# Kernel optimization log

Measured on AMD Instinct MI355X. Metric: run time of the kernel, lower is better.

The kernel has to match this reference:

```python
import math
import jax, jax.numpy as jnp
import numpy as np

UNITS = 256
D_IN = 256
BATCH = 65536
STRENGTH = 0.5
PERIOD = 25.0
LAMBDA_SLOW = 0.1
JITTER = 0.05
H_INERTIA = 0.9
REST_BASELINE = 1.0


def setup_inputs() -> dict:
    key = jax.random.key(0)
    k1, k2, k3, k4, k5, k6 = jax.random.split(key, 6)
    glorot = math.sqrt(2.0 / (D_IN + UNITS))
    return {
        "inputs": jax.random.normal(k1, (BATCH, D_IN), dtype=jnp.float32),
        "prev_h": jax.random.normal(k2, (BATCH, UNITS), dtype=jnp.float32),
        "prev_G": jax.random.normal(k3, (BATCH, UNITS), dtype=jnp.float32),
        "prev_phase": jax.random.normal(k4, (BATCH, 1), dtype=jnp.float32),
        "w_in": jax.random.normal(k5, (D_IN, UNITS), dtype=jnp.float32) * glorot,
        "w_rec": jax.random.normal(k6, (UNITS, UNITS), dtype=jnp.float32) * (1.0 / math.sqrt(UNITS)),
        "bias": jnp.zeros((UNITS,), dtype=jnp.float32),
    }


def reference(inputs, prev_h, prev_G, prev_phase, w_in, w_rec, bias):
    half = UNITS // 2
    # roll-like swap of the two halves of the hidden state
    raw_signal = jnp.concatenate([prev_h[:, half:], prev_h[:, :half]], axis=1)
    # slow exponential-moving-average field
    new_G = (1.0 - LAMBDA_SLOW) * prev_G + LAMBDA_SLOW * raw_signal
    mean = jnp.mean(new_G, axis=-1, keepdims=True)
    std = jnp.std(new_G, axis=-1, keepdims=True)  # population std, matches tf.math.reduce_std
    G_norm = (new_G - mean) / (std + 1e-6)
    new_phase = prev_phase + 2.0 * math.pi / PERIOD
    oscillator = jnp.sin(new_phase)
    bias_signal = jnp.mean(raw_signal, axis=-1, keepdims=True) - 0.1
    combined_signal = oscillator + JITTER * bias_signal
    field_effect = REST_BASELINE + STRENGTH * combined_signal * jnp.tanh(G_norm)
    z = (inputs @ w_in + prev_h @ w_rec + bias) * field_effect
    h = H_INERTIA * prev_h + (1.0 - H_INERTIA) * jax.nn.elu(z)
    h = jnp.clip(h, -20.0, 20.0)
    return (h, new_G, new_phase)
```

## Files before the change

kernel.cpp:

```cpp
#include <hip/hip_runtime.h>

typedef unsigned short ushort_t;
typedef short v8s __attribute__((ext_vector_type(8)));
typedef float v4f __attribute__((ext_vector_type(4)));

#define BATCH    65536
#define UNITS    256
#define M_TILE   32
#define A_PAD    33
#define GT_STRIDE 264
#define LDS_A    0
#define LDS_A_SZ (64 * A_PAD * 16)
#define LDS_GT   LDS_A_SZ
#define LDS_GT_SZ (32 * GT_STRIDE * 2)
#define LDS_SC   (LDS_GT + LDS_GT_SZ)
#define LDS_TOT  (LDS_SC + 1408)

__device__ __forceinline__ float b2f(ushort_t u) {
    union { unsigned int i; float f; } v; v.i = ((unsigned int)u) << 16; return v.f;
}
__device__ __forceinline__ ushort_t f2b(float f) {
    union { float f; unsigned int i; } v; v.f = f;
    unsigned int r = (v.i + 0x7fffu + ((v.i >> 16) & 1u)) >> 16;
    return (ushort_t)r;
}

__global__ void pack_w(const float* __restrict__ w_in,
                       const float* __restrict__ w_rec,
                       ushort_t* __restrict__ Wp) {
    int gid = blockIdx.x * 256 + threadIdx.x;
    int k = gid >> 8, n = gid & 255;
    float v = (k < 256) ? w_in[k * 256 + n] : w_rec[(k - 256) * 256 + n];
    int s = k >> 5, t = n >> 4;
    int lane = ((k >> 3) & 3) * 16 + (n & 15);
    Wp[(size_t)(((s * 16 + t) * 64) + lane) * 8 + (k & 7)] = f2b(v);
}

__global__ __launch_bounds__(256, 3)
void fused_cell(const float* __restrict__ inputs,
                const float* __restrict__ prev_h,
                const float* __restrict__ prev_G,
                const float* __restrict__ prev_phase,
                const ushort_t* __restrict__ Wp,
                const float* __restrict__ bias,
                float* __restrict__ out) {
    __shared__ __align__(16) char smem[LDS_TOT];
    short* Ak     = (short*)(smem + LDS_A);
    short* Gt     = (short*)(smem + LDS_GT);
    float* r_mean = (float*)(smem + LDS_SC);
    float* r_rstd = r_mean + 32;
    float* r_comb = r_rstd + 32;
    float* bias_f = r_comb + 32;

    const int tid  = threadIdx.x;
    const int row0 = blockIdx.x * M_TILE;

    float* outH = out;
    float* outG = out + (size_t)BATCH * UNITS;
    float* outP = out + (size_t)2 * BATCH * UNITS;

    bias_f[tid] = bias[tid];

    {
        const int lr = tid >> 3;
        const int p  = tid & 7;
        const int gr = row0 + lr;
        float s1 = 0.f, s2 = 0.f, sh = 0.f;
        #pragma unroll
        for (int i = 0; i < 8; ++i) {
            int c0 = i * 32 + p * 4;
            int pc = (c0 + 128) & 255;
            float4 xi = *(const float4*)(inputs + (size_t)gr * UNITS + c0);
            float4 hp = *(const float4*)(prev_h + (size_t)gr * UNITS + pc);
            float4 gp = *(const float4*)(prev_G + (size_t)gr * UNITS + c0);
            ushort4 xq; xq.x = f2b(xi.x); xq.y = f2b(xi.y); xq.z = f2b(xi.z); xq.w = f2b(xi.w);
            *(ushort4*)(Ak + ((c0 >> 3) * A_PAD + lr) * 8 + (c0 & 7)) = xq;
            ushort4 hq; hq.x = f2b(hp.x); hq.y = f2b(hp.y); hq.z = f2b(hp.z); hq.w = f2b(hp.w);
            int kh = 256 + pc;
            *(ushort4*)(Ak + ((kh >> 3) * A_PAD + lr) * 8 + (pc & 7)) = hq;
            float4 ng;
            ng.x = 0.9f * gp.x + 0.1f * hp.x;
            ng.y = 0.9f * gp.y + 0.1f * hp.y;
            ng.z = 0.9f * gp.z + 0.1f * hp.z;
            ng.w = 0.9f * gp.w + 0.1f * hp.w;
            s1 += ng.x + ng.y + ng.z + ng.w;
            s2 += ng.x*ng.x + ng.y*ng.y + ng.z*ng.z + ng.w*ng.w;
            sh += hp.x + hp.y + hp.z + hp.w;
            *(float4*)(outG + (size_t)gr * UNITS + c0) = ng;
            ushort4 gq; gq.x = f2b(ng.x); gq.y = f2b(ng.y); gq.z = f2b(ng.z); gq.w = f2b(ng.w);
            *(ushort4*)(Gt + lr * GT_STRIDE + c0) = gq;
        }
        #pragma unroll
        for (int off = 4; off > 0; off >>= 1) {
            s1 += __shfl_xor(s1, off, 64);
            s2 += __shfl_xor(s2, off, 64);
            sh += __shfl_xor(sh, off, 64);
        }
        if (p == 0) {
            float mean = s1 * (1.f / 256.f);
            float var  = s2 * (1.f / 256.f) - mean * mean;
            float rstd = 1.f / (sqrtf(fmaxf(var, 0.f)) + 1e-6f);
            float np   = prev_phase[gr] + 0.2513274122871834591f;
            outP[gr] = np;
            float comb = sinf(np) + 0.05f * (sh * (1.f / 256.f) - 0.1f);
            r_mean[lr] = mean; r_rstd[lr] = rstd; r_comb[lr] = comb;
        }
    }

    __syncthreads();

    const int l   = tid & 63;
    const int w   = tid >> 6;
    const int n16 = l & 15;
    const int q   = l >> 4;

    v4f acc[2][4];
    const v4f z4 = {0.f, 0.f, 0.f, 0.f};
    #pragma unroll
    for (int mi = 0; mi < 2; ++mi)
        #pragma unroll
        for (int t = 0; t < 4; ++t) acc[mi][t] = z4;

    const short* ap = Ak + (q * A_PAD + n16) * 8;
    const short* bw = (const short*)Wp + ((size_t)(w * 4) * 64 + l) * 8;

    #pragma unroll 2
    for (int s = 0; s < 16; ++s) {
        v8s a0 = *(const v8s*)(ap + s * (4 * A_PAD * 8));
        v8s a1 = *(const v8s*)(ap + s * (4 * A_PAD * 8) + 128);
        #pragma unroll
        for (int t = 0; t < 4; ++t) {
            v8s b = *(const v8s*)(bw + (s * 16 + t) * 512);
            acc[0][t] = __builtin_amdgcn_mfma_f32_16x16x32_bf16(a0, b, acc[0][t], 0, 0, 0);
            acc[1][t] = __builtin_amdgcn_mfma_f32_16x16x32_bf16(a1, b, acc[1][t], 0, 0, 0);
        }
    }

    #pragma unroll
    for (int mi = 0; mi < 2; ++mi) {
        #pragma unroll
        for (int t = 0; t < 4; ++t) {
            int c = (w * 4 + t) * 16 + n16;
            float bz = bias_f[c];
            #pragma unroll
            for (int r = 0; r < 4; ++r) {
                int lr = mi * 16 + q * 4 + r;
                int gr = row0 + lr;
                float gval = b2f((ushort_t)Gt[lr * GT_STRIDE + c]);
                float gn = (gval - r_mean[lr]) * r_rstd[lr];
                float e2 = __expf(2.f * gn);
                float th = 1.f - 2.f / (e2 + 1.f);
                float field = 1.f + 0.5f * r_comb[lr] * th;
                float z = (acc[mi][t][r] + bz) * field;
                float el = (z > 0.f) ? z : (__expf(z) - 1.f);
                int kh = 256 + c;
                float hprev = b2f((ushort_t)Ak[((kh >> 3) * A_PAD + lr) * 8 + (c & 7)]);
                float h = 0.9f * hprev + 0.1f * el;
                h = fminf(fmaxf(h, -20.f), 20.f);
                outH[(size_t)gr * UNITS + c] = h;
            }
        }
    }
}

extern "C" void kernel_launch(void* const* d_in, const int* in_sizes, int n_in,
                              void* d_out, int out_size, void* d_ws, size_t ws_size,
                              hipStream_t stream) {
    const float* inputs     = (const float*)d_in[0];
    const float* prev_h     = (const float*)d_in[1];
    const float* prev_G     = (const float*)d_in[2];
    const float* prev_phase = (const float*)d_in[3];
    const float* w_in       = (const float*)d_in[4];
    const float* w_rec      = (const float*)d_in[5];
    const float* bias       = (const float*)d_in[6];
    float* out    = (float*)d_out;
    ushort_t* Wp  = (ushort_t*)d_ws;

    pack_w<<<512, 256, 0, stream>>>(w_in, w_rec, Wp);
    fused_cell<<<BATCH / M_TILE, 256, 0, stream>>>(inputs, prev_h, prev_G,
                                                   prev_phase, Wp, bias, out);
}
```

Before: 318.1 us.

## Load input activations directly into MFMA registers and shrink LDS A buffer

The input-activation half of the A operand is no longer staged through LDS. Each lane loads fp32 inputs from global memory straight into the MFMA fragment layout, converts them to bf16 in registers, and prefetches the first input and weight fragments before the prologue. This halves the A staging buffer in LDS, so occupancy can rise to 4 blocks per CU, and it removes the LDS write/read traffic for that half. The outputs are now written with nontemporal stores. In exchange, the per-lane global loads of inputs are less coalesced (32-byte chunks spread across rows), the fully unrolled loop adds register pressure, and bf16 conversion now happens inside the MFMA loop.

Measured after the change: 317.2 us. About the same (-0.3%).

```diff
diff --git a/kernel.cpp b/kernel.cpp
--- a/kernel.cpp
+++ b/kernel.cpp
@@ -9,9 +9,9 @@
 #define M_TILE   32
 #define A_PAD    33
 #define GT_STRIDE 264
-#define LDS_A    0
-#define LDS_A_SZ (64 * A_PAD * 16)
-#define LDS_GT   LDS_A_SZ
+#define LDS_AK   0
+#define LDS_AK_SZ (32 * A_PAD * 16)
+#define LDS_GT   LDS_AK_SZ
 #define LDS_GT_SZ (32 * GT_STRIDE * 2)
 #define LDS_SC   (LDS_GT + LDS_GT_SZ)
 #define LDS_TOT  (LDS_SC + 1408)
@@ -36,7 +36,7 @@
     Wp[(size_t)(((s * 16 + t) * 64) + lane) * 8 + (k & 7)] = f2b(v);
 }
 
-__global__ __launch_bounds__(256, 3)
+__global__ __launch_bounds__(256, 4)
 void fused_cell(const float* __restrict__ inputs,
                 const float* __restrict__ prev_h,
                 const float* __restrict__ prev_G,
@@ -45,7 +45,7 @@
                 const float* __restrict__ bias,
                 float* __restrict__ out) {
     __shared__ __align__(16) char smem[LDS_TOT];
-    short* Ak     = (short*)(smem + LDS_A);
+    short* Ak     = (short*)(smem + LDS_AK);
     short* Gt     = (short*)(smem + LDS_GT);
     float* r_mean = (float*)(smem + LDS_SC);
     float* r_rstd = r_mean + 32;
@@ -61,6 +61,23 @@
 
     bias_f[tid] = bias[tid];
 
+    const int l   = tid & 63;
+    const int w   = tid >> 6;
+    const int n16 = l & 15;
+    const int q   = l >> 4;
+
+    const float* ainp0 = inputs + (size_t)(row0 + n16) * UNITS + q * 8;
+    const float* ainp1 = ainp0 + 16 * UNITS;
+    const short* bw    = (const short*)Wp + ((size_t)(w * 4) * 64 + l) * 8;
+
+    float4 pA00 = *(const float4*)(ainp0);
+    float4 pA01 = *(const float4*)(ainp0 + 4);
+    float4 pA10 = *(const float4*)(ainp1);
+    float4 pA11 = *(const float4*)(ainp1 + 4);
+    v8s pB[4];
+    #pragma unroll
+    for (int tt = 0; tt < 4; ++tt) pB[tt] = *(const v8s*)(bw + tt * 512);
+
     {
         const int lr = tid >> 3;
         const int p  = tid & 7;
@@ -70,14 +87,8 @@
         for (int i = 0; i < 8; ++i) {
             int c0 = i * 32 + p * 4;
             int pc = (c0 + 128) & 255;
-            float4 xi = *(const float4*)(inputs + (size_t)gr * UNITS + c0);
             float4 hp = *(const float4*)(prev_h + (size_t)gr * UNITS + pc);
             float4 gp = *(const float4*)(prev_G + (size_t)gr * UNITS + c0);
-            ushort4 xq; xq.x = f2b(xi.x); xq.y = f2b(xi.y); xq.z = f2b(xi.z); xq.w = f2b(xi.w);
-            *(ushort4*)(Ak + ((c0 >> 3) * A_PAD + lr) * 8 + (c0 & 7)) = xq;
-            ushort4 hq; hq.x = f2b(hp.x); hq.y = f2b(hp.y); hq.z = f2b(hp.z); hq.w = f2b(hp.w);
-            int kh = 256 + pc;
-            *(ushort4*)(Ak + ((kh >> 3) * A_PAD + lr) * 8 + (pc & 7)) = hq;
             float4 ng;
             ng.x = 0.9f * gp.x + 0.1f * hp.x;
             ng.y = 0.9f * gp.y + 0.1f * hp.y;
@@ -86,9 +97,12 @@
             s1 += ng.x + ng.y + ng.z + ng.w;
             s2 += ng.x*ng.x + ng.y*ng.y + ng.z*ng.z + ng.w*ng.w;
             sh += hp.x + hp.y + hp.z + hp.w;
-            *(float4*)(outG + (size_t)gr * UNITS + c0) = ng;
+            v4f ngv; ngv[0] = ng.x; ngv[1] = ng.y; ngv[2] = ng.z; ngv[3] = ng.w;
+            __builtin_nontemporal_store(ngv, (v4f*)(outG + (size_t)gr * UNITS + c0));
             ushort4 gq; gq.x = f2b(ng.x); gq.y = f2b(ng.y); gq.z = f2b(ng.z); gq.w = f2b(ng.w);
             *(ushort4*)(Gt + lr * GT_STRIDE + c0) = gq;
+            ushort4 hq; hq.x = f2b(hp.x); hq.y = f2b(hp.y); hq.z = f2b(hp.z); hq.w = f2b(hp.w);
+            *(ushort4*)(Ak + ((pc >> 3) * A_PAD + lr) * 8 + (pc & 7)) = hq;
         }
         #pragma unroll
         for (int off = 4; off > 0; off >>= 1) {
@@ -101,7 +115,7 @@
             float var  = s2 * (1.f / 256.f) - mean * mean;
             float rstd = 1.f / (sqrtf(fmaxf(var, 0.f)) + 1e-6f);
             float np   = prev_phase[gr] + 0.2513274122871834591f;
-            outP[gr] = np;
+            __builtin_nontemporal_store(np, outP + gr);
             float comb = sinf(np) + 0.05f * (sh * (1.f / 256.f) - 0.1f);
             r_mean[lr] = mean; r_rstd[lr] = rstd; r_comb[lr] = comb;
         }
@@ -109,38 +123,51 @@
 
     __syncthreads();
 
-    const int l   = tid & 63;
-    const int w   = tid >> 6;
-    const int n16 = l & 15;
-    const int q   = l >> 4;
-
     v4f acc[2][4];
     const v4f z4 = {0.f, 0.f, 0.f, 0.f};
     #pragma unroll
     for (int mi = 0; mi < 2; ++mi)
         #pragma unroll
-        for (int t = 0; t < 4; ++t) acc[mi][t] = z4;
-
-    const short* ap = Ak + (q * A_PAD + n16) * 8;
-    const short* bw = (const short*)Wp + ((size_t)(w * 4) * 64 + l) * 8;
-
-    #pragma unroll 2
+        for (int tt = 0; tt < 4; ++tt) acc[mi][tt] = z4;
+
+    #pragma unroll
     for (int s = 0; s < 16; ++s) {
-        v8s a0 = *(const v8s*)(ap + s * (4 * A_PAD * 8));
-        v8s a1 = *(const v8s*)(ap + s * (4 * A_PAD * 8) + 128);
-        #pragma unroll
-        for (int t = 0; t < 4; ++t) {
-            v8s b = *(const v8s*)(bw + (s * 16 + t) * 512);
-            acc[0][t] = __builtin_amdgcn_mfma_f32_16x16x32_bf16(a0, b, acc[0][t], 0, 0, 0);
-            acc[1][t] = __builtin_amdgcn_mfma_f32_16x16x32_bf16(a1, b, acc[1][t], 0, 0, 0);
+        v8s a0, a1;
+        if (s < 8) {
+            float4 f00, f01, f10, f11;
+            if (s == 0) { f00 = pA00; f01 = pA01; f10 = pA10; f11 = pA11; }
+            else {
+                f00 = *(const float4*)(ainp0 + s * 32);
+                f01 = *(const float4*)(ainp0 + s * 32 + 4);
+                f10 = *(const float4*)(ainp1 + s * 32);
+                f11 = *(const float4*)(ainp1 + s * 32 + 4);
+            }
+            a0[0] = (short)f2b(f00.x); a0[1] = (short)f2b(f00.y);
+            a0[2] = (short)f2b(f00.z); a0[3] = (short)f2b(f00.w);
+            a0[4] = (short)f2b(f01.x); a0[5] = (short)f2b(f01.y);
+            a0[6] = (short)f2b(f01.z); a0[7] = (short)f2b(f01.w);
+            a1[0] = (short)f2b(f10.x); a1[1] = (short)f2b(f10.y);
+            a1[2] = (short)f2b(f10.z); a1[3] = (short)f2b(f10.w);
+            a1[4] = (short)f2b(f11.x); a1[5] = (short)f2b(f11.y);
+            a1[6] = (short)f2b(f11.z); a1[7] = (short)f2b(f11.w);
+        } else {
+            const short* ap = Ak + ((s - 8) * 4 + q) * (A_PAD * 8);
+            a0 = *(const v8s*)(ap + n16 * 8);
+            a1 = *(const v8s*)(ap + (16 + n16) * 8);
+        }
+        #pragma unroll
+        for (int tt = 0; tt < 4; ++tt) {
+            v8s b = (s == 0) ? pB[tt] : *(const v8s*)(bw + (s * 16 + tt) * 512);
+            acc[0][tt] = __builtin_amdgcn_mfma_f32_16x16x32_bf16(a0, b, acc[0][tt], 0, 0, 0);
+            acc[1][tt] = __builtin_amdgcn_mfma_f32_16x16x32_bf16(a1, b, acc[1][tt], 0, 0, 0);
         }
     }
 
     #pragma unroll
     for (int mi = 0; mi < 2; ++mi) {
         #pragma unroll
-        for (int t = 0; t < 4; ++t) {
-            int c = (w * 4 + t) * 16 + n16;
+        for (int tt = 0; tt < 4; ++tt) {
+            int c = (w * 4 + tt) * 16 + n16;
             float bz = bias_f[c];
             #pragma unroll
             for (int r = 0; r < 4; ++r) {
@@ -151,13 +178,12 @@
                 float e2 = __expf(2.f * gn);
                 float th = 1.f - 2.f / (e2 + 1.f);
                 float field = 1.f + 0.5f * r_comb[lr] * th;
-                float z = (acc[mi][t][r] + bz) * field;
+                float z = (acc[mi][tt][r] + bz) * field;
                 float el = (z > 0.f) ? z : (__expf(z) - 1.f);
-                int kh = 256 + c;
-                float hprev = b2f((ushort_t)Ak[((kh >> 3) * A_PAD + lr) * 8 + (c & 7)]);
+                float hprev = b2f((ushort_t)Ak[((c >> 3) * A_PAD + lr) * 8 + (c & 7)]);
                 float h = 0.9f * hprev + 0.1f * el;
                 h = fminf(fmaxf(h, -20.f), 20.f);
-                outH[(size_t)gr * UNITS + c] = h;
+                __builtin_nontemporal_store(h, outH + (size_t)gr * UNITS + c);
             }
         }
     }
```
